# Performance work log

Hardware: AMD Instinct MI355X
Metric: run time of the kernel (lower is better)

## Reference

```python
import jax, jax.numpy as jnp
import numpy as np

EMBED = 1024
HEAD = 128

def setup_inputs() -> dict:
    key = jax.random.key(0)
    k1, k2, k3, k4 = jax.random.split(key, 4)
    x = jax.random.normal(k1, (8, 2048, EMBED), dtype=jnp.float32)
    s = 1.0 / np.sqrt(EMBED)
    Wk = jax.random.normal(k2, (EMBED, HEAD), dtype=jnp.float32) * s
    Wq = jax.random.normal(k3, (EMBED, HEAD), dtype=jnp.float32) * s
    Wv = jax.random.normal(k4, (EMBED, HEAD), dtype=jnp.float32) * s
    return {"x": x, "Wk": Wk, "Wq": Wq, "Wv": Wv}

def reference(x, Wk, Wq, Wv):
    # x: [B,T,E]; projections: [B,T,H]
    k = x @ Wk
    q = x @ Wq
    v = x @ Wv
    T = x.shape[1]
    # NOTE: original scales by 1/sqrt(embedding_size), not head_size
    scale = 1.0 / jnp.sqrt(jnp.asarray(EMBED, dtype=x.dtype))
    scores = jnp.einsum('bth,bsh->bts', q, k) * scale  # [B,T,T]
    causal = jnp.tril(jnp.ones((T, T), dtype=bool))
    scores = jnp.where(causal, scores, -jnp.inf)
    attn = jax.nn.softmax(scores, axis=-1)
    return jnp.einsum('bts,bsh->bth', attn, v)
```

## Files before the change

### kernel.cpp

```cpp
#include <hip/hip_runtime.h>
#include <math.h>

typedef short bf16x2 __attribute__((ext_vector_type(2)));
typedef short bf16x4 __attribute__((ext_vector_type(4)));
typedef short bf16x8 __attribute__((ext_vector_type(8)));
typedef float f32x4 __attribute__((ext_vector_type(4)));

#define EMBED 1024
#define HEAD 128
#define BATCH 8
#define SEQ 2048

__device__ __forceinline__ short f2bf(float f) {
  union { float f; unsigned u; } v;
  v.f = f;
  unsigned r = v.u + 0x7fffu + ((v.u >> 16) & 1u);
  return (short)(r >> 16);
}

__device__ __forceinline__ void async_copy16(const void* g, void* l) {
#if __has_builtin(__builtin_amdgcn_global_load_lds)
  __builtin_amdgcn_global_load_lds(
      (const __attribute__((address_space(1))) unsigned int*)g,
      (__attribute__((address_space(3))) unsigned int*)l, 16, 0, 0);
#else
  *(f32x4*)l = *(const f32x4*)g;
#endif
}

__global__ __launch_bounds__(384) void wtrans_kernel(
    const float* __restrict__ Wq, const float* __restrict__ Wk,
    const float* __restrict__ Wv, short* __restrict__ WT3) {
  int kc8 = blockIdx.x;
  int n = threadIdx.x;
  int mtx = n >> 7, h = n & 127;
  const float* W = (mtx == 0) ? Wq : ((mtx == 1) ? Wk : Wv);
  float scale = (mtx == 0) ? (1.4426950408889634f / 32.0f) : 1.0f;
  bf16x8 o;
#pragma unroll
  for (int j = 0; j < 8; j++)
    o[j] = f2bf(W[(size_t)(kc8 * 8 + j) * HEAD + h] * scale);
  *(bf16x8*)&WT3[(size_t)kc8 * 3072 + n * 8] = o;
}

__global__ __launch_bounds__(512, 2) void proj_kernel(
    const float* __restrict__ x, const short* __restrict__ WT3,
    short* __restrict__ q, short* __restrict__ kG, short* __restrict__ vG) {
  __shared__ __align__(16) short As[2][64 * 72];
  __shared__ __align__(16) short Bs[2][24576];
  int tid = threadIdx.x;
  int w = tid >> 6, lane = tid & 63, quad = lane >> 4, sub = lane & 15;
  int mw = w & 1, nw = w >> 1;
  int mt = blockIdx.x;
  int m0 = mt * 64;

  int arow = tid >> 3;
  int akq = (tid & 7) * 8;
  const float* xbase = x + (size_t)(m0 + arow) * EMBED + akq;
  int aoff = arow * 72 + akq;

  int kcg = tid >> 7;
  int n0 = tid & 127;
  int bdst[6];
#pragma unroll
  for (int j = 0; j < 3; j++)
#pragma unroll
    for (int kk = 0; kk < 2; kk++)
      bdst[j * 2 + kk] = ((kcg * 2 + kk) * 384 + j * 128 + n0) * 8;

  f32x4 acc[2][6];
#pragma unroll
  for (int am = 0; am < 2; am++)
#pragma unroll
    for (int an = 0; an < 6; an++) acc[am][an] = (f32x4)(0.0f);

  {
    f32x4 x0 = *(const f32x4*)(xbase + 0);
    f32x4 x1 = *(const f32x4*)(xbase + 4);
    bf16x8 w0;
    w0[0]=f2bf(x0[0]); w0[1]=f2bf(x0[1]); w0[2]=f2bf(x0[2]); w0[3]=f2bf(x0[3]);
    w0[4]=f2bf(x1[0]); w0[5]=f2bf(x1[1]); w0[6]=f2bf(x1[2]); w0[7]=f2bf(x1[3]);
    *(bf16x8*)&As[0][aoff] = w0;
#pragma unroll
    for (int j = 0; j < 6; j++) async_copy16(WT3 + bdst[j], &Bs[0][bdst[j]]);
  }
  f32x4 xr0 = *(const f32x4*)(xbase + 64);
  f32x4 xr1 = *(const f32x4*)(xbase + 68);

  for (int it = 0; it < 16; it++) {
    int cur = it & 1;
    __syncthreads();
    if (it < 15) {
      int nxt = cur ^ 1;
      bf16x8 w0;
      w0[0]=f2bf(xr0[0]); w0[1]=f2bf(xr0[1]); w0[2]=f2bf(xr0[2]); w0[3]=f2bf(xr0[3]);
      w0[4]=f2bf(xr1[0]); w0[5]=f2bf(xr1[1]); w0[6]=f2bf(xr1[2]); w0[7]=f2bf(xr1[3]);
      *(bf16x8*)&As[nxt][aoff] = w0;
      int bsrc = (it + 1) * 24576;
#pragma unroll
      for (int j = 0; j < 6; j++)
        async_copy16(WT3 + bsrc + bdst[j], &Bs[nxt][bdst[j]]);
      if (it < 14) {
        int kb2 = (it + 2) * 64;
        xr0 = *(const f32x4*)(xbase + kb2);
        xr1 = *(const f32x4*)(xbase + kb2 + 4);
      }
    }
#pragma unroll
    for (int ks = 0; ks < 2; ks++) {
      bf16x8 a0 = *(const bf16x8*)&As[cur][(mw * 32 + sub) * 72 + ks * 32 + quad * 8];
      bf16x8 a1 = *(const bf16x8*)&As[cur][(mw * 32 + 16 + sub) * 72 + ks * 32 + quad * 8];
#pragma unroll
      for (int an = 0; an < 6; an++) {
        bf16x8 bf = *(const bf16x8*)&Bs[cur][((ks * 4 + quad) * 384 + nw * 96 + an * 16 + sub) * 8];
        acc[0][an] = __builtin_amdgcn_mfma_f32_16x16x32_bf16(a0, bf, acc[0][an], 0, 0, 0);
        acc[1][an] = __builtin_amdgcn_mfma_f32_16x16x32_bf16(a1, bf, acc[1][an], 0, 0, 0);
      }
    }
  }

#pragma unroll
  for (int am = 0; am < 2; am++)
#pragma unroll
    for (int an = 0; an < 6; an++) {
      int g = nw * 6 + an;
      int hcol = (g & 7) * 16 + sub;
      if (g < 8) {
#pragma unroll
        for (int r = 0; r < 4; r++) {
          int m = m0 + mw * 32 + am * 16 + quad * 4 + r;
          q[(size_t)m * HEAD + hcol] = f2bf(acc[am][an][r]);
        }
      } else if (g < 16) {
        size_t base = (size_t)(mt * 2 + mw) * 4096 + (hcol >> 3) * 256 + (hcol & 7);
#pragma unroll
        for (int r = 0; r < 4; r++)
          kG[base + (am * 16 + quad * 4 + r) * 8] = f2bf(acc[am][an][r]);
      } else {
        bf16x4 pv;
#pragma unroll
        for (int r = 0; r < 4; r++) pv[r] = f2bf(acc[am][an][r]);
        *(bf16x4*)&vG[(size_t)(mt * 2 + mw) * 4096 + (am * 2 + (quad >> 1)) * 1024 +
                      hcol * 8 + (quad & 1) * 4] = pv;
      }
    }
}

__global__ __launch_bounds__(256, 4) void attn_kernel(
    const short* __restrict__ q, const short* __restrict__ kG,
    const short* __restrict__ vG, float* __restrict__ o_acc,
    float* __restrict__ l_acc) {
  __shared__ __align__(16) short Kb[2][4096];
  __shared__ __align__(16) short Vb[2][4096];
  __shared__ __align__(16) short Pb[4][16 * 40];
  int tid = threadIdx.x;
  int w = tid >> 6, lane = tid & 63, quad = lane >> 4, sub = lane & 15;
  int bx = blockIdx.x;
  int b = bx & 7;
  int v = 79 - (bx >> 3);
  int qt, c;
  if (v < 8)       { qt = v;                               c = 0; }
  else if (v < 24) { int i2 = v - 8;  qt = 8  + (i2 >> 1); c = i2 & 1; }
  else if (v < 48) { int i2 = v - 24; qt = 16 + i2 / 3;    c = i2 % 3; }
  else             { int i2 = v - 48; qt = 24 + (i2 >> 2); c = i2 & 3; }
  int q0 = qt * 64;
  int kb0 = c * 512;
  int len = min(512, q0 + 64 - kb0);
  int ntiles = len >> 5;

  const short* kp = kG + (size_t)b * SEQ * HEAD;
  const short* vp = vG + (size_t)b * SEQ * HEAD;
  int cc0 = tid, cc1 = tid + 256;

  bf16x8 qf[4];
  const short* qrow = q + (size_t)(b * SEQ + q0 + w * 16 + sub) * HEAD + quad * 8;
#pragma unroll
  for (int kc = 0; kc < 4; kc++) qf[kc] = *(const bf16x8*)(qrow + kc * 32);

  f32x4 o[8];
#pragma unroll
  for (int h = 0; h < 8; h++) o[h] = (f32x4)(0.0f);
  float l[4] = {0.0f, 0.0f, 0.0f, 0.0f};
  int wrow = q0 + w * 16;
  int qrq = wrow + quad * 4;

  {
    size_t blk = (size_t)(kb0 >> 5) * 4096;
    async_copy16(kp + blk + cc0 * 8, &Kb[0][cc0 * 8]);
    async_copy16(kp + blk + cc1 * 8, &Kb[0][cc1 * 8]);
    async_copy16(vp + blk + cc0 * 8, &Vb[0][cc0 * 8]);
    async_copy16(vp + blk + cc1 * 8, &Vb[0][cc1 * 8]);
  }

  for (int j = 0; j < ntiles; j++) {
    int kb = kb0 + j * 32;
    int cur = j & 1;
    __syncthreads();
    if (j + 1 < ntiles) {
      int nxt = cur ^ 1;
      size_t blk = (size_t)((kb + 32) >> 5) * 4096;
      async_copy16(kp + blk + cc0 * 8, &Kb[nxt][cc0 * 8]);
      async_copy16(kp + blk + cc1 * 8, &Kb[nxt][cc1 * 8]);
      async_copy16(vp + blk + cc0 * 8, &Vb[nxt][cc0 * 8]);
      async_copy16(vp + blk + cc1 * 8, &Vb[nxt][cc1 * 8]);
    }
    f32x4 s0 = (f32x4)(0.0f), s1 = (f32x4)(0.0f);
#pragma unroll
    for (int kk = 0; kk < 4; kk++) {
      bf16x8 f0 = *(const bf16x8*)&Kb[cur][((kk * 4 + quad) * 32 + sub) * 8];
      bf16x8 f1 = *(const bf16x8*)&Kb[cur][((kk * 4 + quad) * 32 + 16 + sub) * 8];
      s0 = __builtin_amdgcn_mfma_f32_16x16x32_bf16(qf[kk], f0, s0, 0, 0, 0);
      s1 = __builtin_amdgcn_mfma_f32_16x16x32_bf16(qf[kk], f1, s1, 0, 0, 0);
    }
    bool edge = (kb + 31 > wrow);
    float e0[4], e1[4];
#pragma unroll
    for (int r = 0; r < 4; r++) {
      e0[r] = __builtin_amdgcn_exp2f(s0[r]);
      e1[r] = __builtin_amdgcn_exp2f(s1[r]);
    }
    if (edge) {
#pragma unroll
      for (int r = 0; r < 4; r++) {
        if (kb + sub > qrq + r) e0[r] = 0.0f;
        if (kb + 16 + sub > qrq + r) e1[r] = 0.0f;
      }
    }
    short* pw = &Pb[w][0];
#pragma unroll
    for (int r = 0; r < 4; r++) {
      l[r] += e0[r] + e1[r];
      pw[(quad * 4 + r) * 40 + sub] = f2bf(e0[r]);
      pw[(quad * 4 + r) * 40 + sub + 16] = f2bf(e1[r]);
    }
    bf16x8 pa = *(const bf16x8*)&pw[sub * 40 + quad * 8];
#pragma unroll
    for (int h8 = 0; h8 < 8; h8++) {
      bf16x8 vf = *(const bf16x8*)&Vb[cur][(quad * 128 + h8 * 16 + sub) * 8];
      o[h8] = __builtin_amdgcn_mfma_f32_16x16x32_bf16(pa, vf, o[h8], 0, 0, 0);
    }
  }

  float* ob = o_acc + (size_t)(b * SEQ + qrq) * HEAD + sub;
#pragma unroll
  for (int r = 0; r < 4; r++)
#pragma unroll
    for (int h8 = 0; h8 < 8; h8++)
      unsafeAtomicAdd(ob + (size_t)r * HEAD + h8 * 16, o[h8][r]);
#pragma unroll
  for (int r = 0; r < 4; r++) {
#pragma unroll
    for (int off = 1; off < 16; off <<= 1) l[r] += __shfl_xor(l[r], off);
  }
  if (sub == 0) {
#pragma unroll
    for (int r = 0; r < 4; r++)
      unsafeAtomicAdd(&l_acc[b * SEQ + qrq + r], l[r]);
  }
}

__global__ __launch_bounds__(256) void norm_kernel(
    float* __restrict__ o, const float* __restrict__ l_acc) {
  int idx = blockIdx.x * 256 + threadIdx.x;
  f32x4 v = ((const f32x4*)o)[idx];
  float inv = 1.0f / l_acc[idx >> 5];
  v[0] *= inv; v[1] *= inv; v[2] *= inv; v[3] *= inv;
  ((f32x4*)o)[idx] = v;
}

extern "C" void kernel_launch(void* const* d_in, const int* in_sizes, int n_in,
                              void* d_out, int out_size, void* d_ws, size_t ws_size,
                              hipStream_t stream) {
  const float* x  = (const float*)d_in[0];
  const float* Wk = (const float*)d_in[1];
  const float* Wq = (const float*)d_in[2];
  const float* Wv = (const float*)d_in[3];
  char* ws = (char*)d_ws;
  short* WT3   = (short*)(ws);
  short* vG    = (short*)(ws + (size_t)1  * (1 << 20));
  short* q     = (short*)(ws + (size_t)5  * (1 << 20));
  short* kG    = (short*)(ws + (size_t)9  * (1 << 20));
  float* l_acc = (float*)(ws + (size_t)13 * (1 << 20));
  float* out   = (float*)d_out;

  hipMemsetAsync(out, 0, (size_t)BATCH * SEQ * HEAD * sizeof(float), stream);
  hipMemsetAsync(l_acc, 0, (size_t)BATCH * SEQ * sizeof(float), stream);
  wtrans_kernel<<<dim3(128), 384, 0, stream>>>(Wq, Wk, Wv, WT3);
  proj_kernel<<<dim3(256), 512, 0, stream>>>(x, WT3, q, kG, vG);
  attn_kernel<<<dim3(640), 256, 0, stream>>>(q, kG, vG, out, l_acc);
  norm_kernel<<<dim3(2048), 256, 0, stream>>>(out, l_acc);
}
```

Measured before the change: 158.3 us.

## Load projection weight fragments directly into registers instead of staging through LDS

The projection kernel stops staging the transposed weight tile in shared memory through async global-to-LDS copies. Each wave now loads its own B fragments straight from global memory into double-buffered registers, one step ahead. The warp tiling also changes from 2x4 to 1x8 (each wave covers all 64 rows and 48 columns), so every wave reads only its own weight columns and A reuse goes up. This removes a large LDS buffer and its LDS reads, in exchange for more global/L2 traffic per wave and higher register pressure from twelve held fragments.

```diff
diff --git a/kernel.cpp b/kernel.cpp
--- a/kernel.cpp
+++ b/kernel.cpp
@@ -43,14 +43,63 @@
   *(bf16x8*)&WT3[(size_t)kc8 * 3072 + n * 8] = o;
 }
 
+#define MFMA_BF16(D, A, B) D = __builtin_amdgcn_mfma_f32_16x16x32_bf16(A, B, D, 0, 0, 0)
+
+#define PROJ_BODY(IT, C0, C1, C2, C3, C4, C5, N0, N1, N2, N3, N4, N5)          \
+  {                                                                            \
+    int it_ = (IT);                                                            \
+    __syncthreads();                                                           \
+    if (it_ < 15) {                                                            \
+      const short* bp_ = bptr + (it_ + 1) * 24576;                             \
+      N0 = *(const bf16x8*)(bp_);                                              \
+      N1 = *(const bf16x8*)(bp_ + 128);                                        \
+      N2 = *(const bf16x8*)(bp_ + 256);                                        \
+      N3 = *(const bf16x8*)(bp_ + 12288);                                      \
+      N4 = *(const bf16x8*)(bp_ + 12288 + 128);                                \
+      N5 = *(const bf16x8*)(bp_ + 12288 + 256);                                \
+      bf16x8 w0_;                                                              \
+      w0_[0] = f2bf(xr0[0]); w0_[1] = f2bf(xr0[1]);                            \
+      w0_[2] = f2bf(xr0[2]); w0_[3] = f2bf(xr0[3]);                            \
+      w0_[4] = f2bf(xr1[0]); w0_[5] = f2bf(xr1[1]);                            \
+      w0_[6] = f2bf(xr1[2]); w0_[7] = f2bf(xr1[3]);                            \
+      *(bf16x8*)&As[(it_ & 1) ^ 1][aoff] = w0_;                                \
+      if (it_ < 14) {                                                          \
+        xr0 = *(const f32x4*)(xbase + (it_ + 2) * 64);                         \
+        xr1 = *(const f32x4*)(xbase + (it_ + 2) * 64 + 4);                     \
+      }                                                                        \
+    }                                                                          \
+    {                                                                          \
+      const short* as_ = &As[it_ & 1][0];                                      \
+      bf16x8 a0_ = *(const bf16x8*)&as_[sub * 72 + quad * 8];                  \
+      bf16x8 a1_ = *(const bf16x8*)&as_[(16 + sub) * 72 + quad * 8];           \
+      bf16x8 a2_ = *(const bf16x8*)&as_[(32 + sub) * 72 + quad * 8];           \
+      bf16x8 a3_ = *(const bf16x8*)&as_[(48 + sub) * 72 + quad * 8];           \
+      MFMA_BF16(acc[0][0], a0_, C0); MFMA_BF16(acc[1][0], a1_, C0);            \
+      MFMA_BF16(acc[2][0], a2_, C0); MFMA_BF16(acc[3][0], a3_, C0);            \
+      MFMA_BF16(acc[0][1], a0_, C1); MFMA_BF16(acc[1][1], a1_, C1);            \
+      MFMA_BF16(acc[2][1], a2_, C1); MFMA_BF16(acc[3][1], a3_, C1);            \
+      MFMA_BF16(acc[0][2], a0_, C2); MFMA_BF16(acc[1][2], a1_, C2);            \
+      MFMA_BF16(acc[2][2], a2_, C2); MFMA_BF16(acc[3][2], a3_, C2);            \
+      a0_ = *(const bf16x8*)&as_[sub * 72 + 32 + quad * 8];                    \
+      a1_ = *(const bf16x8*)&as_[(16 + sub) * 72 + 32 + quad * 8];             \
+      a2_ = *(const bf16x8*)&as_[(32 + sub) * 72 + 32 + quad * 8];             \
+      a3_ = *(const bf16x8*)&as_[(48 + sub) * 72 + 32 + quad * 8];             \
+      MFMA_BF16(acc[0][0], a0_, C3); MFMA_BF16(acc[1][0], a1_, C3);            \
+      MFMA_BF16(acc[2][0], a2_, C3); MFMA_BF16(acc[3][0], a3_, C3);            \
+      MFMA_BF16(acc[0][1], a0_, C4); MFMA_BF16(acc[1][1], a1_, C4);            \
+      MFMA_BF16(acc[2][1], a2_, C4); MFMA_BF16(acc[3][1], a3_, C4);            \
+      MFMA_BF16(acc[0][2], a0_, C5); MFMA_BF16(acc[1][2], a1_, C5);            \
+      MFMA_BF16(acc[2][2], a2_, C5); MFMA_BF16(acc[3][2], a3_, C5);            \
+    }                                                                          \
+  }
+
 __global__ __launch_bounds__(512, 2) void proj_kernel(
     const float* __restrict__ x, const short* __restrict__ WT3,
     short* __restrict__ q, short* __restrict__ kG, short* __restrict__ vG) {
   __shared__ __align__(16) short As[2][64 * 72];
-  __shared__ __align__(16) short Bs[2][24576];
   int tid = threadIdx.x;
   int w = tid >> 6, lane = tid & 63, quad = lane >> 4, sub = lane & 15;
-  int mw = w & 1, nw = w >> 1;
+  int nw = w;
   int mt = blockIdx.x;
   int m0 = mt * 64;
 
@@ -59,20 +108,13 @@
   const float* xbase = x + (size_t)(m0 + arow) * EMBED + akq;
   int aoff = arow * 72 + akq;
 
-  int kcg = tid >> 7;
-  int n0 = tid & 127;
-  int bdst[6];
-#pragma unroll
-  for (int j = 0; j < 3; j++)
-#pragma unroll
-    for (int kk = 0; kk < 2; kk++)
-      bdst[j * 2 + kk] = ((kcg * 2 + kk) * 384 + j * 128 + n0) * 8;
-
-  f32x4 acc[2][6];
-#pragma unroll
-  for (int am = 0; am < 2; am++)
-#pragma unroll
-    for (int an = 0; an < 6; an++) acc[am][an] = (f32x4)(0.0f);
+  const short* bptr = WT3 + quad * 3072 + nw * 384 + sub * 8;
+
+  f32x4 acc[4][3];
+#pragma unroll
+  for (int am = 0; am < 4; am++)
+#pragma unroll
+    for (int an = 0; an < 3; an++) acc[am][an] = (f32x4)(0.0f);
 
   {
     f32x4 x0 = *(const f32x4*)(xbase + 0);
@@ -81,66 +123,46 @@
     w0[0]=f2bf(x0[0]); w0[1]=f2bf(x0[1]); w0[2]=f2bf(x0[2]); w0[3]=f2bf(x0[3]);
     w0[4]=f2bf(x1[0]); w0[5]=f2bf(x1[1]); w0[6]=f2bf(x1[2]); w0[7]=f2bf(x1[3]);
     *(bf16x8*)&As[0][aoff] = w0;
-#pragma unroll
-    for (int j = 0; j < 6; j++) async_copy16(WT3 + bdst[j], &Bs[0][bdst[j]]);
   }
   f32x4 xr0 = *(const f32x4*)(xbase + 64);
   f32x4 xr1 = *(const f32x4*)(xbase + 68);
-
-  for (int it = 0; it < 16; it++) {
-    int cur = it & 1;
-    __syncthreads();
-    if (it < 15) {
-      int nxt = cur ^ 1;
-      bf16x8 w0;
-      w0[0]=f2bf(xr0[0]); w0[1]=f2bf(xr0[1]); w0[2]=f2bf(xr0[2]); w0[3]=f2bf(xr0[3]);
-      w0[4]=f2bf(xr1[0]); w0[5]=f2bf(xr1[1]); w0[6]=f2bf(xr1[2]); w0[7]=f2bf(xr1[3]);
-      *(bf16x8*)&As[nxt][aoff] = w0;
-      int bsrc = (it + 1) * 24576;
-#pragma unroll
-      for (int j = 0; j < 6; j++)
-        async_copy16(WT3 + bsrc + bdst[j], &Bs[nxt][bdst[j]]);
-      if (it < 14) {
-        int kb2 = (it + 2) * 64;
-        xr0 = *(const f32x4*)(xbase + kb2);
-        xr1 = *(const f32x4*)(xbase + kb2 + 4);
-      }
-    }
-#pragma unroll
-    for (int ks = 0; ks < 2; ks++) {
-      bf16x8 a0 = *(const bf16x8*)&As[cur][(mw * 32 + sub) * 72 + ks * 32 + quad * 8];
-      bf16x8 a1 = *(const bf16x8*)&As[cur][(mw * 32 + 16 + sub) * 72 + ks * 32 + quad * 8];
-#pragma unroll
-      for (int an = 0; an < 6; an++) {
-        bf16x8 bf = *(const bf16x8*)&Bs[cur][((ks * 4 + quad) * 384 + nw * 96 + an * 16 + sub) * 8];
-        acc[0][an] = __builtin_amdgcn_mfma_f32_16x16x32_bf16(a0, bf, acc[0][an], 0, 0, 0);
-        acc[1][an] = __builtin_amdgcn_mfma_f32_16x16x32_bf16(a1, bf, acc[1][an], 0, 0, 0);
-      }
-    }
-  }
-
-#pragma unroll
-  for (int am = 0; am < 2; am++)
-#pragma unroll
-    for (int an = 0; an < 6; an++) {
-      int g = nw * 6 + an;
+  bf16x8 bA0, bA1, bA2, bA3, bA4, bA5;
+  bf16x8 bB0, bB1, bB2, bB3, bB4, bB5;
+  bA0 = *(const bf16x8*)(bptr);
+  bA1 = *(const bf16x8*)(bptr + 128);
+  bA2 = *(const bf16x8*)(bptr + 256);
+  bA3 = *(const bf16x8*)(bptr + 12288);
+  bA4 = *(const bf16x8*)(bptr + 12288 + 128);
+  bA5 = *(const bf16x8*)(bptr + 12288 + 256);
+
+  for (int it2 = 0; it2 < 16; it2 += 2) {
+    PROJ_BODY(it2,     bA0, bA1, bA2, bA3, bA4, bA5, bB0, bB1, bB2, bB3, bB4, bB5);
+    PROJ_BODY(it2 + 1, bB0, bB1, bB2, bB3, bB4, bB5, bA0, bA1, bA2, bA3, bA4, bA5);
+  }
+
+#pragma unroll
+  for (int am = 0; am < 4; am++)
+#pragma unroll
+    for (int an = 0; an < 3; an++) {
+      int g = nw * 3 + an;
       int hcol = (g & 7) * 16 + sub;
       if (g < 8) {
 #pragma unroll
         for (int r = 0; r < 4; r++) {
-          int m = m0 + mw * 32 + am * 16 + quad * 4 + r;
+          int m = m0 + am * 16 + quad * 4 + r;
           q[(size_t)m * HEAD + hcol] = f2bf(acc[am][an][r]);
         }
       } else if (g < 16) {
-        size_t base = (size_t)(mt * 2 + mw) * 4096 + (hcol >> 3) * 256 + (hcol & 7);
+        size_t base = (size_t)(mt * 2 + (am >> 1)) * 4096 + (hcol >> 3) * 256 + (hcol & 7);
 #pragma unroll
         for (int r = 0; r < 4; r++)
-          kG[base + (am * 16 + quad * 4 + r) * 8] = f2bf(acc[am][an][r]);
+          kG[base + ((am & 1) * 16 + quad * 4 + r) * 8] = f2bf(acc[am][an][r]);
       } else {
         bf16x4 pv;
 #pragma unroll
         for (int r = 0; r < 4; r++) pv[r] = f2bf(acc[am][an][r]);
-        *(bf16x4*)&vG[(size_t)(mt * 2 + mw) * 4096 + (am * 2 + (quad >> 1)) * 1024 +
+        *(bf16x4*)&vG[(size_t)(mt * 2 + (am >> 1)) * 4096 +
+                      ((am & 1) * 2 + (quad >> 1)) * 1024 +
                       hcol * 8 + (quad & 1) * 4] = pv;
       }
     }
```

Measured after the change: 158.2 us. Within noise of the previous version (-0.1%).
